# Kernel tuning notes

Measured on AMD Instinct MI355X. Metric: run time of the kernel, lower is better.

Reference implementation:

```python
import jax, jax.numpy as jnp
import numpy as np

C, INTER, RED4 = 256, 128, 64  # in_channels, inter_ch=max(C//2,32), C//4

def setup_inputs() -> dict:
    key = jax.random.key(0)
    ks = jax.random.split(key, 12)
    B, H, W = 8, 64, 64
    s = 0.02
    return {
        "x": jax.random.normal(ks[0], (B, C, H, W), dtype=jnp.float32),
        "theta_w": jax.random.normal(ks[1], (INTER, C), dtype=jnp.float32) * s,
        "phi_w": jax.random.normal(ks[2], (INTER, C), dtype=jnp.float32) * s,
        "g_w": jax.random.normal(ks[3], (INTER, C), dtype=jnp.float32) * s,
        "out_w": jax.random.normal(ks[4], (C, INTER), dtype=jnp.float32) * s,
        "bn_gamma": jnp.ones((C,), dtype=jnp.float32),
        "bn_beta": jnp.zeros((C,), dtype=jnp.float32),
        "fc1_w": jax.random.normal(ks[5], (RED4, C), dtype=jnp.float32) * s,
        "fc1_b": jnp.zeros((RED4,), dtype=jnp.float32),
        "fc2_w": jax.random.normal(ks[6], (C, RED4), dtype=jnp.float32) * s,
        "fc2_b": jnp.zeros((C,), dtype=jnp.float32),
    }

def reference(x, theta_w, phi_w, g_w, out_w, bn_gamma, bn_beta, fc1_w, fc1_b, fc2_w, fc2_b):
    B, Cc, H, W = x.shape
    N = H * W
    xf = x.reshape(B, Cc, N)                              # [B,C,N]
    # 1x1 convs == per-pixel matmuls
    theta = jnp.einsum('ic,bcn->bni', theta_w, xf)        # [B,N,I]
    phi = jnp.einsum('ic,bcn->bin', phi_w, xf)            # [B,I,N]
    g = jnp.einsum('ic,bcn->bni', g_w, xf)                # [B,N,I]
    scale = 1.0 / jnp.sqrt(jnp.asarray(theta.shape[-1], theta.dtype))
    attn = jax.nn.softmax(jnp.einsum('bni,bim->bnm', theta, phi) * scale, axis=-1)  # [B,N,N]
    out = jnp.einsum('bnm,bmi->bni', attn, g)             # [B,N,I]
    out = jnp.einsum('ci,bni->bcn', out_w, out).reshape(B, Cc, H, W)
    # BatchNorm2d (training mode: batch stats, biased variance, eps=1e-5)
    mean = out.mean(axis=(0, 2, 3))
    var = out.var(axis=(0, 2, 3))
    out = (out - mean[:, None, None]) * jax.lax.rsqrt(var[:, None, None] + 1e-5)
    out = out * bn_gamma[:, None, None] + bn_beta[:, None, None]
    # SE channel attention on the input x
    pooled = x.mean(axis=(2, 3))                          # [B,C]
    h = jax.nn.relu(pooled @ fc1_w.T + fc1_b)
    ch_w = jax.nn.sigmoid(h @ fc2_w.T + fc2_b)[:, :, None, None]
    return x + out * ch_w
```

## Files before the change

### kernel.cpp

```cpp
#include <hip/hip_runtime.h>

#define B_DIM 8
#define C_DIM 256
#define I_DIM 128
#define N_DIM 4096
#define R_DIM 64

typedef unsigned short u16;
typedef unsigned int u32;
typedef __attribute__((ext_vector_type(8))) __bf16 bf16x8;
typedef __attribute__((ext_vector_type(4))) float f32x4;
typedef __attribute__((ext_vector_type(16))) float f32x16;

union BF8 { u32 u[4]; bf16x8 v; };

__device__ __forceinline__ u16 f2bf(float f) {
    union { float f; u32 u; } v; v.f = f;
    u32 r = v.u + 0x7FFFu + ((v.u >> 16) & 1u);
    return (u16)(r >> 16);
}
__device__ __forceinline__ float bf2f(u16 h) {
    union { u32 u; float f; } v; v.u = (u32)h << 16; return v.f;
}
__device__ __forceinline__ u32 pk2(float a, float b) {
    return (u32)f2bf(a) | ((u32)f2bf(b) << 16);
}
__device__ __forceinline__ u32 pk2t(float a, float b) {
    union { float f; u32 u; } ua, ub; ua.f = a; ub.f = b;
    return __builtin_amdgcn_perm(ub.u, ua.u, 0x07060302u);
}
__device__ __forceinline__ void async16(const u16* g, u16* l) {
    __builtin_amdgcn_global_load_lds((const __attribute__((address_space(1))) void*)g,
                                     (__attribute__((address_space(3))) void*)l, 16, 0, 0);
}

#define TH_SCALE 0.1275204890136f

static constexpr size_t OFF_BNSUM = 0;
static constexpr size_t OFF_BNSQ  = 1024;
static constexpr size_t OFF_POOL  = 2048;
static constexpr size_t OFF_CHW   = 10240;
static constexpr size_t OFF_W3    = 18432;
static constexpr size_t OFF_OWB   = 215040;
static constexpr size_t OFF_AO0   = 280576;
static constexpr size_t OFF_AO1   = OFF_AO0 + 8388608;
static constexpr size_t OFF_THETA = OFF_AO1 + 8388608;
static constexpr size_t OFF_PHIT  = OFF_THETA + 8388608;
static constexpr size_t OFF_GT    = OFF_PHIT + 8388608;
static constexpr size_t OFF_L0    = OFF_GT + 8388608;
static constexpr size_t OFF_L1    = OFF_L0 + 131072;
static constexpr size_t OFF_OUT2  = OFF_L1 + 131072;

__global__ void prep_kernel(const float* __restrict__ tw, const float* __restrict__ pw,
                            const float* __restrict__ gw, const float* __restrict__ ow,
                            u16* __restrict__ w3, u16* __restrict__ owb,
                            float* __restrict__ bnzero, float* __restrict__ pooled) {
    int idx = blockIdx.x * 256 + threadIdx.x;
    if (idx < 512) bnzero[idx] = 0.f;
    if (idx < 2048) pooled[idx] = 0.f;
    if (idx < 3 * 32768) {
        const float* src = idx < 32768 ? tw : (idx < 65536 ? pw : gw);
        w3[idx] = f2bf(src[idx & 32767]);
    }
    if (idx < 32768) owb[idx] = f2bf(ow[idx]);
}

__global__ void se_kernel(const float* __restrict__ pooled,
                          const float* __restrict__ fc1w, const float* __restrict__ fc1b,
                          const float* __restrict__ fc2w, const float* __restrict__ fc2b,
                          float* __restrict__ chw) {
    int b = blockIdx.x, t = threadIdx.x;
    __shared__ float sp[C_DIM], sh[R_DIM];
    sp[t] = pooled[b * C_DIM + t] * (1.f / N_DIM);
    __syncthreads();
    if (t < R_DIM) {
        float a = fc1b[t];
        for (int c = 0; c < C_DIM; ++c) a += sp[c] * fc1w[t * C_DIM + c];
        sh[t] = a > 0.f ? a : 0.f;
    }
    __syncthreads();
    float a = fc2b[t];
    for (int j = 0; j < R_DIM; ++j) a += sh[j] * fc2w[t * R_DIM + j];
    chw[b * C_DIM + t] = 1.f / (1.f + __builtin_amdgcn_exp2f(-a * 1.44269504089f));
}

__global__ __launch_bounds__(256) void qkv_kernel(const float* __restrict__ x,
                                                  const u16* __restrict__ w3,
                                                  u16* __restrict__ theta,
                                                  u16* __restrict__ phiT,
                                                  u16* __restrict__ gT,
                                                  float* __restrict__ pooled) {
    const int bid = blockIdx.x;
    const int b = bid & 7, nt = bid >> 3;
    const int n0 = nt * 64;
    const int t = threadIdx.x, lane = t & 63, w = t >> 6;
    const int cl = lane & 31, h = lane >> 5;

    __shared__ u16 As[64 * 256];
    __shared__ u16 Ep[128 * 72];

    {
        const float* xb = x + ((size_t)b * C_DIM) * N_DIM + n0;
        for (int it = 0; it < 16; ++it) {
            int id = it * 256 + t;
            int c = id >> 4, l16 = id & 15;
            float4 v = *(const float4*)(xb + (size_t)c * N_DIM + l16 * 4);
            int g = c >> 3, co = c & 7;
            float vv[4] = {v.x, v.y, v.z, v.w};
            #pragma unroll
            for (int k = 0; k < 4; ++k) {
                int n = l16 * 4 + k;
                As[n * 256 + ((g ^ (n & 7)) << 3) + co] = f2bf(vv[k]);
            }
            float s = (v.x + v.y) + (v.z + v.w);
            s += __shfl_xor(s, 1); s += __shfl_xor(s, 2);
            s += __shfl_xor(s, 4); s += __shfl_xor(s, 8);
            if ((t & 15) == 0) atomicAdd(&pooled[b * C_DIM + c], s);
        }
    }
    __syncthreads();

    const int mt = w & 1;
    const int ip = w >> 1;
    bf16x8 afr[16];
    #pragma unroll
    for (int ks = 0; ks < 16; ++ks) {
        int r = mt * 32 + cl;
        int g = 2 * ks + h;
        afr[ks] = *(const bf16x8*)&As[r * 256 + ((g ^ (r & 7)) << 3)];
    }

    for (int z = 0; z < 3; ++z) {
        const u16* wz = w3 + z * (I_DIM * C_DIM);
        f32x16 acc[2] = {};
        #pragma unroll
        for (int ks = 0; ks < 16; ++ks) {
            #pragma unroll
            for (int f = 0; f < 2; ++f) {
                int irow = (2 * ip + f) * 32 + cl;
                bf16x8 bfr = *(const bf16x8*)(wz + (size_t)irow * C_DIM + ks * 16 + h * 8);
                acc[f] = __builtin_amdgcn_mfma_f32_32x32x16_bf16(afr[ks], bfr, acc[f], 0, 0, 0);
            }
        }
        if (z < 2) {
            float sc = (z == 0) ? TH_SCALE : 1.0f;
            #pragma unroll
            for (int f = 0; f < 2; ++f) {
                int i = (2 * ip + f) * 32 + cl;
                #pragma unroll
                for (int r2 = 0; r2 < 4; ++r2)
                    #pragma unroll
                    for (int e = 0; e < 4; ++e) {
                        int n = mt * 32 + 8 * r2 + 4 * h + e;
                        Ep[n * 136 + i] = f2bf(acc[f][4 * r2 + e] * sc);
                    }
            }
            __syncthreads();
            u16* dst = (z == 0) ? theta : phiT;
            #pragma unroll
            for (int it = 0; it < 4; ++it) {
                int id = it * 256 + t;
                int n = id >> 4, l16 = id & 15;
                f32x4 vv = *(const f32x4*)&Ep[n * 136 + l16 * 8];
                *(f32x4*)(dst + ((size_t)(b * N_DIM) + n0 + n) * I_DIM + l16 * 8) = vv;
            }
            __syncthreads();
        } else {
            #pragma unroll
            for (int f = 0; f < 2; ++f) {
                int i = (2 * ip + f) * 32 + cl;
                #pragma unroll
                for (int r2 = 0; r2 < 4; ++r2) {
                    u32 lo = pk2(acc[f][4 * r2 + 0], acc[f][4 * r2 + 1]);
                    u32 hi = pk2(acc[f][4 * r2 + 2], acc[f][4 * r2 + 3]);
                    int nb = mt * 32 + 8 * r2 + 4 * h;
                    *(u32*)&Ep[i * 72 + nb] = lo;
                    *(u32*)&Ep[i * 72 + nb + 2] = hi;
                }
            }
            __syncthreads();
            #pragma unroll
            for (int it = 0; it < 4; ++it) {
                int id = it * 256 + t;
                int i = id >> 3, l8 = id & 7;
                f32x4 vv = *(const f32x4*)&Ep[i * 72 + l8 * 8];
                *(f32x4*)(gT + ((size_t)(b * I_DIM) + i) * N_DIM + n0 + l8 * 8) = vv;
            }
        }
    }
}

__global__ __launch_bounds__(256) void attn_kernel(const u16* __restrict__ theta,
                                                   const u16* __restrict__ phiT,
                                                   const u16* __restrict__ gT,
                                                   u16* __restrict__ ao0, u16* __restrict__ ao1,
                                                   float* __restrict__ l0, float* __restrict__ l1) {
    const int bid = blockIdx.x;
    const int b = bid & 7, mh = (bid >> 3) & 1, qt = bid >> 4;
    const int t = threadIdx.x, lane = t & 63, w = t >> 6;
    const int cl = lane & 31, h = lane >> 5;
    const int qw = qt * 128 + w * 32;

    __shared__ u16 SM[32768];
    __shared__ float lex[4][32];

    bf16x8 qf[8];
    {
        const u16* qp = theta + ((size_t)(b * N_DIM) + qw + cl) * I_DIM + h * 8;
        #pragma unroll
        for (int ks = 0; ks < 8; ++ks) qf[ks] = *(const bf16x8*)(qp + ks * 16);
    }

    const u16* kbase = phiT + (size_t)b * N_DIM * I_DIM + (size_t)(mh * 2048) * I_DIM;
    const u16* vbase = gT + (size_t)b * I_DIM * N_DIM + mh * 2048;
    const u16* kptr[4]; const u16* vptr[4];
    #pragma unroll
    for (int it = 0; it < 4; ++it) {
        int gi = (w * 4 + it) * 64 + lane;
        int kr = gi >> 4, kg = gi & 15;
        kptr[it] = kbase + (size_t)kr * I_DIM + ((kg ^ (kr & 7)) << 3);
        int vr = gi >> 3, vg = gi & 7;
        vptr[it] = vbase + (size_t)vr * N_DIM + ((vg ^ (vr & 7)) << 3);
    }

    auto issue = [&](int p) {
        u16* Kd = SM + p * 16384;
        u16* Vd = SM + p * 16384 + 8192;
        #pragma unroll
        for (int it = 0; it < 4; ++it) { async16(kptr[it], Kd + (w * 4 + it) * 512); kptr[it] += 64 * I_DIM; }
        #pragma unroll
        for (int it = 0; it < 4; ++it) { async16(vptr[it], Vd + (w * 4 + it) * 512); vptr[it] += 64; }
    };

    float lsum = 0.f;
    f32x16 O[4] = {};

    issue(0);

    for (int mc = 0; mc < 32; ++mc) {
        const int p = mc & 1;
        __asm__ volatile("s_barrier" ::: "memory");
        if (mc < 31) {
            issue(1 - p);
            __asm__ volatile("s_waitcnt vmcnt(8)" ::: "memory");
        } else {
            __asm__ volatile("s_waitcnt vmcnt(0)" ::: "memory");
        }
        __asm__ volatile("s_barrier" ::: "memory");

        const u16* Ks = SM + p * 16384;
        const u16* Vs = SM + p * 16384 + 8192;

        u32 pk[8][2];
        #pragma unroll
        for (int mt2 = 0; mt2 < 2; ++mt2) {
            f32x16 S = {};
            #pragma unroll
            for (int ks = 0; ks < 8; ++ks) {
                int r = mt2 * 32 + cl;
                bf16x8 kf = *(const bf16x8*)&Ks[r * 128 + (((2 * ks + h) ^ (r & 7)) << 3)];
                S = __builtin_amdgcn_mfma_f32_32x32x16_bf16(kf, qf[ks], S, 0, 0, 0);
            }
            #pragma unroll
            for (int r2 = 0; r2 < 4; ++r2) {
                float p0 = __builtin_amdgcn_exp2f(S[4 * r2 + 0]);
                float p1 = __builtin_amdgcn_exp2f(S[4 * r2 + 1]);
                float p2 = __builtin_amdgcn_exp2f(S[4 * r2 + 2]);
                float p3 = __builtin_amdgcn_exp2f(S[4 * r2 + 3]);
                lsum += (p0 + p1) + (p2 + p3);
                pk[mt2 * 4 + r2][0] = pk2t(p0, p1);
                pk[mt2 * 4 + r2][1] = pk2t(p2, p3);
            }
        }

        #pragma unroll
        for (int ks = 0; ks < 4; ++ks) {
            u32 a0 = pk[2 * ks][0], a1 = pk[2 * ks][1];
            u32 b0 = pk[2 * ks + 1][0], b1 = pk[2 * ks + 1][1];
            bool hb = (h != 0);
            u32 own0 = hb ? b0 : a0, own1 = hb ? b1 : a1;
            u32 xf0 = hb ? a0 : b0, xf1 = hb ? a1 : b1;
            u32 rc0 = (u32)__shfl_xor((int)xf0, 32);
            u32 rc1 = (u32)__shfl_xor((int)xf1, 32);
            BF8 A;
            A.u[0] = hb ? rc0 : own0;
            A.u[1] = hb ? rc1 : own1;
            A.u[2] = hb ? own0 : rc0;
            A.u[3] = hb ? own1 : rc1;
            #pragma unroll
            for (int f = 0; f < 4; ++f) {
                int ir = f * 32 + cl;
                bf16x8 vf = *(const bf16x8*)&Vs[ir * 64 + (((2 * ks + h) ^ (ir & 7)) << 3)];
                O[f] = __builtin_amdgcn_mfma_f32_32x32x16_bf16(A.v, vf, O[f], 0, 0, 0);
            }
        }
    }

    lsum += __shfl_xor(lsum, 32);
    if (h == 0) lex[w][cl] = lsum;
    __asm__ volatile("s_waitcnt lgkmcnt(0)" ::: "memory");

    float linv[16];
    {
        float* lw = lex[w];
        #pragma unroll
        for (int r2 = 0; r2 < 4; ++r2) {
            f32x4 lv = *(const f32x4*)&lw[8 * r2 + 4 * h];
            #pragma unroll
            for (int e = 0; e < 4; ++e) linv[4 * r2 + e] = 1.f / lv[e];
        }
    }

    u16* aop = (mh == 0) ? ao0 : ao1;
    float* lp = (mh == 0) ? l0 : l1;
    if (h == 0) lp[(size_t)b * N_DIM + qw + cl] = lsum;

    u16* ep = SM + w * 4096;
    #pragma unroll
    for (int f = 0; f < 4; ++f)
        #pragma unroll
        for (int r2 = 0; r2 < 4; ++r2)
            #pragma unroll
            for (int e = 0; e < 4; ++e) {
                int q = 8 * r2 + 4 * h + e;
                ep[q * 128 + f * 32 + cl] = f2bf(O[f][4 * r2 + e] * linv[4 * r2 + e]);
            }
    __asm__ volatile("s_waitcnt lgkmcnt(0)" ::: "memory");
    #pragma unroll
    for (int it = 0; it < 8; ++it) {
        int id = it * 64 + lane;
        int q = id >> 4, l16 = id & 15;
        f32x4 vv = *(const f32x4*)&ep[q * 128 + l16 * 8];
        *(f32x4*)(aop + ((size_t)(b * N_DIM) + qw + q) * I_DIM + l16 * 8) = vv;
    }
}

__global__ __launch_bounds__(256) void oproj_kernel(const u16* __restrict__ ao0,
                                                    const u16* __restrict__ ao1,
                                                    const float* __restrict__ l0,
                                                    const float* __restrict__ l1,
                                                    const u16* __restrict__ owb,
                                                    u16* __restrict__ out2,
                                                    float* __restrict__ bnsum,
                                                    float* __restrict__ bnsumsq) {
    const int bid = blockIdx.x;
    const int b = bid & 7, nt = bid >> 3;
    const int n0 = nt * 64;
    const int t = threadIdx.x, lane = t & 63, w = t >> 6;
    const int cl = lane & 31, h = lane >> 5;

    __shared__ u16 Ep[256 * 72];
    __shared__ float lsum[C_DIM], lsq[C_DIM];
    lsum[t] = 0.f; lsq[t] = 0.f;
    __syncthreads();

    const int mt = w & 1;
    const int nn = n0 + mt * 32 + cl;
    float w0, w1;
    {
        float la = l0[(size_t)b * N_DIM + nn], lb = l1[(size_t)b * N_DIM + nn];
        float inv = 1.f / (la + lb);
        w0 = la * inv; w1 = lb * inv;
    }
    bf16x8 afr[8];
    {
        const u16* p0 = ao0 + ((size_t)(b * N_DIM) + nn) * I_DIM + h * 8;
        const u16* p1 = ao1 + ((size_t)(b * N_DIM) + nn) * I_DIM + h * 8;
        #pragma unroll
        for (int ks = 0; ks < 8; ++ks) {
            bf16x8 x0 = *(const bf16x8*)(p0 + ks * 16);
            bf16x8 x1 = *(const bf16x8*)(p1 + ks * 16);
            const u16* u0 = (const u16*)&x0;
            const u16* u1 = (const u16*)&x1;
            float c0 = w0 * bf2f(u0[0]) + w1 * bf2f(u1[0]);
            float c1 = w0 * bf2f(u0[1]) + w1 * bf2f(u1[1]);
            float c2 = w0 * bf2f(u0[2]) + w1 * bf2f(u1[2]);
            float c3 = w0 * bf2f(u0[3]) + w1 * bf2f(u1[3]);
            float c4 = w0 * bf2f(u0[4]) + w1 * bf2f(u1[4]);
            float c5 = w0 * bf2f(u0[5]) + w1 * bf2f(u1[5]);
            float c6 = w0 * bf2f(u0[6]) + w1 * bf2f(u1[6]);
            float c7 = w0 * bf2f(u0[7]) + w1 * bf2f(u1[7]);
            BF8 r;
            r.u[0] = pk2(c0, c1); r.u[1] = pk2(c2, c3);
            r.u[2] = pk2(c4, c5); r.u[3] = pk2(c6, c7);
            afr[ks] = r.v;
        }
    }

    f32x16 D[4] = {};
    #pragma unroll
    for (int ks = 0; ks < 8; ++ks) {
        #pragma unroll
        for (int j = 0; j < 4; ++j) {
            int cr = ((w >> 1) * 4 + j) * 32 + cl;
            bf16x8 bfr = *(const bf16x8*)(owb + (size_t)cr * I_DIM + ks * 16 + h * 8);
            D[j] = __builtin_amdgcn_mfma_f32_32x32x16_bf16(afr[ks], bfr, D[j], 0, 0, 0);
        }
    }

    #pragma unroll
    for (int j = 0; j < 4; ++j) {
        int c = ((w >> 1) * 4 + j) * 32 + cl;
        float s1 = 0.f, s2 = 0.f;
        #pragma unroll
        for (int r2 = 0; r2 < 4; ++r2) {
            float v0 = D[j][4 * r2 + 0], v1 = D[j][4 * r2 + 1];
            float v2 = D[j][4 * r2 + 2], v3 = D[j][4 * r2 + 3];
            s1 += (v0 + v1) + (v2 + v3);
            s2 += (v0 * v0 + v1 * v1) + (v2 * v2 + v3 * v3);
            int nb = mt * 32 + 8 * r2 + 4 * h;
            *(u32*)&Ep[c * 72 + nb] = pk2(v0, v1);
            *(u32*)&Ep[c * 72 + nb + 2] = pk2(v2, v3);
        }
        atomicAdd(&lsum[c], s1);
        atomicAdd(&lsq[c], s2);
    }
    __syncthreads();
    #pragma unroll
    for (int it = 0; it < 8; ++it) {
        int id = it * 256 + t;
        int c = id >> 3, l8 = id & 7;
        f32x4 vv = *(const f32x4*)&Ep[c * 72 + l8 * 8];
        *(f32x4*)(out2 + ((size_t)(b * C_DIM) + c) * N_DIM + n0 + l8 * 8) = vv;
    }
    atomicAdd(&bnsum[t], lsum[t]);
    atomicAdd(&bnsumsq[t], lsq[t]);
}

__global__ void final_kernel(const float* __restrict__ x, const u16* __restrict__ out2,
                             const float* __restrict__ bnsum, const float* __restrict__ bnsumsq,
                             const float* __restrict__ gamma, const float* __restrict__ beta,
                             const float* __restrict__ chw, float* __restrict__ out) {
    int idx = blockIdx.x * 256 + threadIdx.x;
    int e = idx * 4;
    int b = e >> 20;
    int c = (e >> 12) & 255;
    float mean = bnsum[c] * (1.f / 32768.f);
    float var = bnsumsq[c] * (1.f / 32768.f) - mean * mean;
    float sc = gamma[c] * rsqrtf(var + 1e-5f);
    float sh = beta[c] - mean * sc;
    float cw = chw[b * C_DIM + c];
    ushort4 o16 = ((const ushort4*)out2)[idx];
    float4 xv = ((const float4*)x)[idx];
    float4 res;
    res.x = xv.x + (bf2f(o16.x) * sc + sh) * cw;
    res.y = xv.y + (bf2f(o16.y) * sc + sh) * cw;
    res.z = xv.z + (bf2f(o16.z) * sc + sh) * cw;
    res.w = xv.w + (bf2f(o16.w) * sc + sh) * cw;
    ((float4*)out)[idx] = res;
}

extern "C" void kernel_launch(void* const* d_in, const int* in_sizes, int n_in,
                              void* d_out, int out_size, void* d_ws, size_t ws_size,
                              hipStream_t stream) {
    const float* x   = (const float*)d_in[0];
    const float* tw  = (const float*)d_in[1];
    const float* pw  = (const float*)d_in[2];
    const float* gw  = (const float*)d_in[3];
    const float* ow  = (const float*)d_in[4];
    const float* gam = (const float*)d_in[5];
    const float* bet = (const float*)d_in[6];
    const float* f1w = (const float*)d_in[7];
    const float* f1b = (const float*)d_in[8];
    const float* f2w = (const float*)d_in[9];
    const float* f2b = (const float*)d_in[10];
    float* out = (float*)d_out;

    char* ws = (char*)d_ws;
    float* bnsum   = (float*)(ws + OFF_BNSUM);
    float* bnsumsq = (float*)(ws + OFF_BNSQ);
    float* pooled  = (float*)(ws + OFF_POOL);
    float* chw     = (float*)(ws + OFF_CHW);
    u16*   w3      = (u16*)(ws + OFF_W3);
    u16*   owb     = (u16*)(ws + OFF_OWB);
    u16*   ao0     = (u16*)(ws + OFF_AO0);
    u16*   ao1     = (u16*)(ws + OFF_AO1);
    u16*   theta   = (u16*)(ws + OFF_THETA);
    u16*   phiT    = (u16*)(ws + OFF_PHIT);
    u16*   gT      = (u16*)(ws + OFF_GT);
    float* l0      = (float*)(ws + OFF_L0);
    float* l1      = (float*)(ws + OFF_L1);
    u16*   out2    = (u16*)(ws + OFF_OUT2);

    prep_kernel<<<384, 256, 0, stream>>>(tw, pw, gw, ow, w3, owb, bnsum, pooled);
    qkv_kernel<<<512, 256, 0, stream>>>(x, w3, theta, phiT, gT, pooled);
    se_kernel<<<B_DIM, 256, 0, stream>>>(pooled, f1w, f1b, f2w, f2b, chw);
    attn_kernel<<<512, 256, 0, stream>>>(theta, phiT, gT, ao0, ao1, l0, l1);
    oproj_kernel<<<512, 256, 0, stream>>>(ao0, ao1, l0, l1, owb, out2, bnsum, bnsumsq);
    final_kernel<<<8192, 256, 0, stream>>>(x, out2, bnsum, bnsumsq, gam, bet, chw, out);
}
```

Baseline: 270.4 us.

## Process two query tiles per wave in attention kernel to reuse K/V fragments

Each wave now handles 64 query rows instead of 32, so every K and V fragment loaded from shared memory feeds two MFMA chains. This halves the K/V global-to-LDS traffic per query and the grid shrinks from 512 to 256 blocks. In exchange, register pressure roughly doubles for the O accumulators and Q fragments, which may reduce occupancy, and 256 blocks may underfill the GPU's compute units.

```diff
diff --git a/kernel.cpp b/kernel.cpp
--- a/kernel.cpp
+++ b/kernel.cpp
@@ -199,16 +199,17 @@
     const int b = bid & 7, mh = (bid >> 3) & 1, qt = bid >> 4;
     const int t = threadIdx.x, lane = t & 63, w = t >> 6;
     const int cl = lane & 31, h = lane >> 5;
-    const int qw = qt * 128 + w * 32;
+    const int qw = qt * 256 + w * 64;
 
     __shared__ u16 SM[32768];
-    __shared__ float lex[4][32];
-
-    bf16x8 qf[8];
-    {
-        const u16* qp = theta + ((size_t)(b * N_DIM) + qw + cl) * I_DIM + h * 8;
-        #pragma unroll
-        for (int ks = 0; ks < 8; ++ks) qf[ks] = *(const bf16x8*)(qp + ks * 16);
+    __shared__ float lex[4][64];
+
+    bf16x8 qf[2][8];
+    #pragma unroll
+    for (int qi = 0; qi < 2; ++qi) {
+        const u16* qp = theta + ((size_t)(b * N_DIM) + qw + qi * 32 + cl) * I_DIM + h * 8;
+        #pragma unroll
+        for (int ks = 0; ks < 8; ++ks) qf[qi][ks] = *(const bf16x8*)(qp + ks * 16);
     }
 
     const u16* kbase = phiT + (size_t)b * N_DIM * I_DIM + (size_t)(mh * 2048) * I_DIM;
@@ -232,8 +233,8 @@
         for (int it = 0; it < 4; ++it) { async16(vptr[it], Vd + (w * 4 + it) * 512); vptr[it] += 64; }
     };
 
-    float lsum = 0.f;
-    f32x16 O[4] = {};
+    float lsum[2] = {0.f, 0.f};
+    f32x16 O[2][4] = {};
 
     issue(0);
 
@@ -251,83 +252,99 @@
         const u16* Ks = SM + p * 16384;
         const u16* Vs = SM + p * 16384 + 8192;
 
-        u32 pk[8][2];
         #pragma unroll
         for (int mt2 = 0; mt2 < 2; ++mt2) {
-            f32x16 S = {};
+            bf16x8 kf[8];
             #pragma unroll
             for (int ks = 0; ks < 8; ++ks) {
                 int r = mt2 * 32 + cl;
-                bf16x8 kf = *(const bf16x8*)&Ks[r * 128 + (((2 * ks + h) ^ (r & 7)) << 3)];
-                S = __builtin_amdgcn_mfma_f32_32x32x16_bf16(kf, qf[ks], S, 0, 0, 0);
-            }
-            #pragma unroll
-            for (int r2 = 0; r2 < 4; ++r2) {
-                float p0 = __builtin_amdgcn_exp2f(S[4 * r2 + 0]);
-                float p1 = __builtin_amdgcn_exp2f(S[4 * r2 + 1]);
-                float p2 = __builtin_amdgcn_exp2f(S[4 * r2 + 2]);
-                float p3 = __builtin_amdgcn_exp2f(S[4 * r2 + 3]);
-                lsum += (p0 + p1) + (p2 + p3);
-                pk[mt2 * 4 + r2][0] = pk2t(p0, p1);
-                pk[mt2 * 4 + r2][1] = pk2t(p2, p3);
-            }
-        }
-
-        #pragma unroll
-        for (int ks = 0; ks < 4; ++ks) {
-            u32 a0 = pk[2 * ks][0], a1 = pk[2 * ks][1];
-            u32 b0 = pk[2 * ks + 1][0], b1 = pk[2 * ks + 1][1];
-            bool hb = (h != 0);
-            u32 own0 = hb ? b0 : a0, own1 = hb ? b1 : a1;
-            u32 xf0 = hb ? a0 : b0, xf1 = hb ? a1 : b1;
-            u32 rc0 = (u32)__shfl_xor((int)xf0, 32);
-            u32 rc1 = (u32)__shfl_xor((int)xf1, 32);
-            BF8 A;
-            A.u[0] = hb ? rc0 : own0;
-            A.u[1] = hb ? rc1 : own1;
-            A.u[2] = hb ? own0 : rc0;
-            A.u[3] = hb ? own1 : rc1;
-            #pragma unroll
-            for (int f = 0; f < 4; ++f) {
-                int ir = f * 32 + cl;
-                bf16x8 vf = *(const bf16x8*)&Vs[ir * 64 + (((2 * ks + h) ^ (ir & 7)) << 3)];
-                O[f] = __builtin_amdgcn_mfma_f32_32x32x16_bf16(A.v, vf, O[f], 0, 0, 0);
-            }
-        }
-    }
-
-    lsum += __shfl_xor(lsum, 32);
-    if (h == 0) lex[w][cl] = lsum;
-    __asm__ volatile("s_waitcnt lgkmcnt(0)" ::: "memory");
-
-    float linv[16];
-    {
-        float* lw = lex[w];
+                kf[ks] = *(const bf16x8*)&Ks[r * 128 + (((2 * ks + h) ^ (r & 7)) << 3)];
+            }
+            u32 pkq[2][4][2];
+            #pragma unroll
+            for (int qi = 0; qi < 2; ++qi) {
+                f32x16 S = {};
+                #pragma unroll
+                for (int ks = 0; ks < 8; ++ks)
+                    S = __builtin_amdgcn_mfma_f32_32x32x16_bf16(kf[ks], qf[qi][ks], S, 0, 0, 0);
+                #pragma unroll
+                for (int r2 = 0; r2 < 4; ++r2) {
+                    float p0 = __builtin_amdgcn_exp2f(S[4 * r2 + 0]);
+                    float p1 = __builtin_amdgcn_exp2f(S[4 * r2 + 1]);
+                    float p2 = __builtin_amdgcn_exp2f(S[4 * r2 + 2]);
+                    float p3 = __builtin_amdgcn_exp2f(S[4 * r2 + 3]);
+                    lsum[qi] += (p0 + p1) + (p2 + p3);
+                    pkq[qi][r2][0] = pk2t(p0, p1);
+                    pkq[qi][r2][1] = pk2t(p2, p3);
+                }
+            }
+            #pragma unroll
+            for (int l = 0; l < 2; ++l) {
+                const int gks = 2 * mt2 + l;
+                BF8 A[2];
+                #pragma unroll
+                for (int qi = 0; qi < 2; ++qi) {
+                    u32 a0 = pkq[qi][2 * l][0], a1 = pkq[qi][2 * l][1];
+                    u32 b0 = pkq[qi][2 * l + 1][0], b1 = pkq[qi][2 * l + 1][1];
+                    bool hb = (h != 0);
+                    u32 own0 = hb ? b0 : a0, own1 = hb ? b1 : a1;
+                    u32 xf0 = hb ? a0 : b0, xf1 = hb ? a1 : b1;
+                    u32 rc0 = (u32)__shfl_xor((int)xf0, 32);
+                    u32 rc1 = (u32)__shfl_xor((int)xf1, 32);
+                    A[qi].u[0] = hb ? rc0 : own0;
+                    A[qi].u[1] = hb ? rc1 : own1;
+                    A[qi].u[2] = hb ? own0 : rc0;
+                    A[qi].u[3] = hb ? own1 : rc1;
+                }
+                #pragma unroll
+                for (int f = 0; f < 4; ++f) {
+                    int ir = f * 32 + cl;
+                    bf16x8 vf = *(const bf16x8*)&Vs[ir * 64 + (((2 * gks + h) ^ (ir & 7)) << 3)];
+                    O[0][f] = __builtin_amdgcn_mfma_f32_32x32x16_bf16(A[0].v, vf, O[0][f], 0, 0, 0);
+                    O[1][f] = __builtin_amdgcn_mfma_f32_32x32x16_bf16(A[1].v, vf, O[1][f], 0, 0, 0);
+                }
+            }
+        }
+    }
+
+    lsum[0] += __shfl_xor(lsum[0], 32);
+    lsum[1] += __shfl_xor(lsum[1], 32);
+    if (h == 0) { lex[w][cl] = lsum[0]; lex[w][32 + cl] = lsum[1]; }
+    __syncthreads();
+
+    float linv[2][16];
+    #pragma unroll
+    for (int qi = 0; qi < 2; ++qi) {
         #pragma unroll
         for (int r2 = 0; r2 < 4; ++r2) {
-            f32x4 lv = *(const f32x4*)&lw[8 * r2 + 4 * h];
-            #pragma unroll
-            for (int e = 0; e < 4; ++e) linv[4 * r2 + e] = 1.f / lv[e];
+            f32x4 lv = *(const f32x4*)&lex[w][qi * 32 + 8 * r2 + 4 * h];
+            #pragma unroll
+            for (int e = 0; e < 4; ++e) linv[qi][4 * r2 + e] = 1.f / lv[e];
         }
     }
 
     u16* aop = (mh == 0) ? ao0 : ao1;
     float* lp = (mh == 0) ? l0 : l1;
-    if (h == 0) lp[(size_t)b * N_DIM + qw + cl] = lsum;
-
-    u16* ep = SM + w * 4096;
-    #pragma unroll
-    for (int f = 0; f < 4; ++f)
-        #pragma unroll
-        for (int r2 = 0; r2 < 4; ++r2)
-            #pragma unroll
-            for (int e = 0; e < 4; ++e) {
-                int q = 8 * r2 + 4 * h + e;
-                ep[q * 128 + f * 32 + cl] = f2bf(O[f][4 * r2 + e] * linv[4 * r2 + e]);
-            }
+    if (h == 0) {
+        lp[(size_t)b * N_DIM + qw + cl] = lsum[0];
+        lp[(size_t)b * N_DIM + qw + 32 + cl] = lsum[1];
+    }
+
+    u16* ep = SM + w * 8192;
+    #pragma unroll
+    for (int qi = 0; qi < 2; ++qi)
+        #pragma unroll
+        for (int f = 0; f < 4; ++f)
+            #pragma unroll
+            for (int r2 = 0; r2 < 4; ++r2)
+                #pragma unroll
+                for (int e = 0; e < 4; ++e) {
+                    int q = qi * 32 + 8 * r2 + 4 * h + e;
+                    ep[q * 128 + f * 32 + cl] = f2bf(O[qi][f][4 * r2 + e] * linv[qi][4 * r2 + e]);
+                }
     __asm__ volatile("s_waitcnt lgkmcnt(0)" ::: "memory");
     #pragma unroll
-    for (int it = 0; it < 8; ++it) {
+    for (int it = 0; it < 16; ++it) {
         int id = it * 64 + lane;
         int q = id >> 4, l16 = id & 15;
         f32x4 vv = *(const f32x4*)&ep[q * 128 + l16 * 8];
@@ -485,7 +502,7 @@
     prep_kernel<<<384, 256, 0, stream>>>(tw, pw, gw, ow, w3, owb, bnsum, pooled);
     qkv_kernel<<<512, 256, 0, stream>>>(x, w3, theta, phiT, gT, pooled);
     se_kernel<<<B_DIM, 256, 0, stream>>>(pooled, f1w, f1b, f2w, f2b, chw);
-    attn_kernel<<<512, 256, 0, stream>>>(theta, phiT, gT, ao0, ao1, l0, l1);
+    attn_kernel<<<256, 256, 0, stream>>>(theta, phiT, gT, ao0, ao1, l0, l1);
     oproj_kernel<<<512, 256, 0, stream>>>(ao0, ao1, l0, l1, owb, out2, bnsum, bnsumsq);
     final_kernel<<<8192, 256, 0, stream>>>(x, out2, bnsum, bnsumsq, gam, bet, chw, out);
 }
```

Result: slower. 290.2 us (+7.3%).
